# Kernel optimization log

Measured on AMD Instinct MI355X. Metric: run time of the kernel, lower is better.

Reference implementation:

```python
import jax, jax.numpy as jnp
import numpy as np

N_LVL = 127.0   # 8-bit symmetric: 2**(8-1) - 1
BN_EPS = 1e-5
PATCH = 16


def quant_act(x):
    """Per-tensor 8-bit symmetric quant-dequant (HAWQ-style QuantAct, dynamic range)."""
    scale = jnp.max(jnp.abs(x)) / N_LVL
    xq = jnp.clip(jnp.round(x / scale), -N_LVL, N_LVL) * scale
    return xq, scale


def setup_inputs() -> dict:
    key = jax.random.key(0)
    k0, k1, k2, k3, k4 = jax.random.split(key, 5)
    B, C, H = 128, 3, 224
    dim = 768
    x = jax.random.normal(k0, (B, C, H, H), jnp.float32)
    W = jax.random.normal(k1, (dim, C, PATCH, PATCH), jnp.float32) * 0.02
    b = jax.random.normal(k2, (dim,), jnp.float32) * 0.02
    gamma = jnp.ones((dim,), jnp.float32)
    beta = jnp.zeros((dim,), jnp.float32)
    run_mean = jax.random.normal(k3, (dim,), jnp.float32) * 0.1
    run_var = jax.random.uniform(k4, (dim,), jnp.float32, 0.5, 1.5)
    return {"x": x, "W": W, "b": b, "gamma": gamma, "beta": beta,
            "run_mean": run_mean, "run_var": run_var}


def reference(x, W, b, gamma, beta, run_mean, run_var):
    # --- quant_input ---
    x_q, pre_s = quant_act(x)                                   # [B,3,224,224], scalar
    # --- QuantConv2d: per-out-channel 8-bit symmetric weight quant ---
    w_scale = jnp.max(jnp.abs(W), axis=(1, 2, 3), keepdims=True) / N_LVL  # [dim,1,1,1]
    w_int = jnp.round(W / w_scale)
    x_int = x_q / pre_s                                         # integer-valued activations
    comb_s = w_scale[:, 0, 0, 0] * pre_s                        # [dim] conv output scale
    b_int = jnp.round(b / comb_s)
    y = jax.lax.conv_general_dilated(
        x_int, w_int, window_strides=(PATCH, PATCH), padding='VALID',
        dimension_numbers=('NCHW', 'OIHW', 'NCHW'))             # [B,768,14,14]
    y = (y + b_int[None, :, None, None]) * comb_s[None, :, None, None]
    # --- quant_act_conv ---
    y, _ = quant_act(y)
    # --- GELU (torch nn.GELU default: exact erf) ---
    y = jax.nn.gelu(y, approximate=False)
    # --- qact1 ---
    y, _ = quant_act(y)
    # --- BatchNorm2d (eval mode, running stats) ---
    inv = gamma / jnp.sqrt(run_var + BN_EPS)
    y = y * inv[None, :, None, None] + (beta - run_mean * inv)[None, :, None, None]
    # --- qact2 ---
    y, act_scale = quant_act(y)
    return y, act_scale
```

## Files before the change

kernel.cpp:

```cpp
#include <hip/hip_runtime.h>

#define TOT   19267584
#define MROWS 25088
#define KD    768
#define NPB   196
#define CHW   150528

typedef unsigned int uint;
typedef __attribute__((ext_vector_type(4))) int i32x4;

#define OFF_AQ   0ull
#define OFF_WQ   19267584ull
#define OFF_WSC  19857408ull
#define OFF_INV  19860480ull
#define OFF_SHF  19863552ull
#define OFF_CMN  19866624ull
#define OFF_CMX  19869696ull
#define OFF_SC   19872768ull

__device__ __forceinline__ float wave_max(float v) {
#pragma unroll
  for (int off = 32; off > 0; off >>= 1) v = fmaxf(v, __shfl_xor(v, off));
  return v;
}

__device__ __forceinline__ void block_max_atomic(float v, uint* dst) {
  __shared__ float red[4];
  v = wave_max(v);
  const int lane = threadIdx.x & 63, wv = threadIdx.x >> 6;
  if (lane == 0) red[wv] = v;
  __syncthreads();
  if (threadIdx.x == 0)
    atomicMax(dst, __float_as_uint(fmaxf(fmaxf(red[0], red[1]), fmaxf(red[2], red[3]))));
}

__global__ void k_maxabs(const float* __restrict__ x, uint* __restrict__ sc) {
  float m = 0.f;
  const float4* x4 = (const float4*)x;
  for (int i = blockIdx.x * blockDim.x + threadIdx.x; i < TOT / 4; i += gridDim.x * blockDim.x) {
    float4 v = x4[i];
    m = fmaxf(m, fmaxf(fmaxf(fabsf(v.x), fabsf(v.y)), fmaxf(fabsf(v.z), fabsf(v.w))));
  }
  block_max_atomic(m, sc + 0);
}

__global__ void k_wquant(const float* __restrict__ W, const float* __restrict__ gamma,
                         const float* __restrict__ beta, const float* __restrict__ rmean,
                         const float* __restrict__ rvar, signed char* __restrict__ wq,
                         float* __restrict__ wscale, float* __restrict__ inv_,
                         float* __restrict__ shf) {
  const int oc = blockIdx.x;
  const float* row = W + oc * KD;
  float m = 0.f;
  for (int k = threadIdx.x; k < KD; k += 256) m = fmaxf(m, fabsf(row[k]));
  __shared__ float red[4];
  m = wave_max(m);
  if ((threadIdx.x & 63) == 0) red[threadIdx.x >> 6] = m;
  __syncthreads();
  const float ws_ = fmaxf(fmaxf(red[0], red[1]), fmaxf(red[2], red[3])) / 127.0f;
  for (int k = threadIdx.x; k < KD; k += 256)
    wq[oc * KD + k] = (signed char)(int)rintf(row[k] / ws_);
  if (threadIdx.x == 0) {
    wscale[oc] = ws_;
    float iv = gamma[oc] / sqrtf(rvar[oc] + 1e-5f);
    inv_[oc] = iv;
    shf[oc] = __fsub_rn(beta[oc], __fmul_rn(rmean[oc], iv));
  }
}

__global__ void k_im2col(const float* __restrict__ x, const uint* __restrict__ sc,
                         signed char* __restrict__ aq) {
  const float ps = __uint_as_float(sc[0]) / 127.0f;
  char4* a4 = (char4*)aq;
  for (int u = blockIdx.x * blockDim.x + threadIdx.x; u < TOT / 4; u += gridDim.x * blockDim.x) {
    int p = u / 192;
    int k = (u - p * 192) * 4;
    int c = k >> 8;
    int r = k & 255;
    int kh = r >> 4, kw = r & 15;
    int b = p / NPB;
    int pp = p - b * NPB;
    int ph = pp / 14;
    int pw = pp - ph * 14;
    float4 v = *(const float4*)(x + (((b * 3 + c) * 224 + ph * 16 + kh) * 224 + pw * 16 + kw));
    char4 o;
    o.x = (signed char)(int)fminf(fmaxf(rintf(v.x / ps), -127.f), 127.f);
    o.y = (signed char)(int)fminf(fmaxf(rintf(v.y / ps), -127.f), 127.f);
    o.z = (signed char)(int)fminf(fmaxf(rintf(v.z / ps), -127.f), 127.f);
    o.w = (signed char)(int)fminf(fmaxf(rintf(v.w / ps), -127.f), 127.f);
    a4[u] = o;
  }
}

__device__ __forceinline__ void gl_lds16(const void* g, void* l) {
  __builtin_amdgcn_global_load_lds((const __attribute__((address_space(1))) void*)g,
                                   (__attribute__((address_space(3))) void*)l, 16, 0, 0);
}

__global__ __launch_bounds__(256) void k_gemm(const signed char* __restrict__ aq,
                                              const signed char* __restrict__ wq,
                                              const float* __restrict__ bias,
                                              const float* __restrict__ wscale,
                                              uint* __restrict__ sc,
                                              float* __restrict__ y) {
  __shared__ __align__(16) signed char lA[2][8192];
  __shared__ __align__(16) signed char lB[2][8192];
  const int tid = threadIdx.x, lane = tid & 63, wv = tid >> 6;
  const int bsw = (blockIdx.x & 7) * 147 + (blockIdx.x >> 3);
  const int bm = bsw / 6, bn = bsw - 6 * (bsw / 6);
  const int wr = wv >> 1, wc = wv & 1;
  const float ps = __uint_as_float(sc[0]) / 127.0f;

  const int ci0 = wv * 2, ci1 = wv * 2 + 1;
  const int rr0 = ci0 * 16 + (lane >> 2);
  const int rr1 = ci1 * 16 + (lane >> 2);
  const int bo = (lane & 3) * 16;
  const signed char* gA0 = aq + (size_t)(bm * 128 + rr0) * KD + bo;
  const signed char* gA1 = aq + (size_t)(bm * 128 + rr1) * KD + bo;
  const signed char* gB0 = wq + (size_t)(bn * 128 + rr0) * KD + bo;
  const signed char* gB1 = wq + (size_t)(bn * 128 + rr1) * KD + bo;

  i32x4 acc[4][4];
#pragma unroll
  for (int m = 0; m < 4; ++m)
#pragma unroll
    for (int n = 0; n < 4; ++n) acc[m][n] = (i32x4){0, 0, 0, 0};

  const int rbase = lane & 15;
  const int kg = (lane >> 4) * 16;

  gl_lds16(gA0, &lA[0][ci0 * 1024]);
  gl_lds16(gA1, &lA[0][ci1 * 1024]);
  gl_lds16(gB0, &lB[0][ci0 * 1024]);
  gl_lds16(gB1, &lB[0][ci1 * 1024]);
  __syncthreads();

  int cur = 0;
  for (int t = 0; t < 12; ++t) {
    if (t < 11) {
      const int kk = (t + 1) * 64;
      gl_lds16(gA0 + kk, &lA[cur ^ 1][ci0 * 1024]);
      gl_lds16(gA1 + kk, &lA[cur ^ 1][ci1 * 1024]);
      gl_lds16(gB0 + kk, &lB[cur ^ 1][ci0 * 1024]);
      gl_lds16(gB1 + kk, &lB[cur ^ 1][ci1 * 1024]);
    }
    i32x4 af[4], bfr[4];
#pragma unroll
    for (int m = 0; m < 4; ++m)
      af[m] = *(const i32x4*)&lA[cur][(wr * 64 + m * 16 + rbase) * 64 + kg];
#pragma unroll
    for (int n = 0; n < 4; ++n)
      bfr[n] = *(const i32x4*)&lB[cur][(wc * 64 + n * 16 + rbase) * 64 + kg];
#pragma unroll
    for (int m = 0; m < 4; ++m)
#pragma unroll
      for (int n = 0; n < 4; ++n)
        acc[m][n] = __builtin_amdgcn_mfma_i32_16x16x64_i8(af[m], bfr[n], acc[m][n], 0, 0, 0);
    __syncthreads();
    cur ^= 1;
  }

  float lmax = 0.f;
  const int prow = (lane >> 4) << 2;
#pragma unroll
  for (int n = 0; n < 4; ++n) {
    const int oc = bn * 128 + wc * 64 + n * 16 + rbase;
    const float comb = wscale[oc] * ps;
    const float bint = rintf(bias[oc] / comb);
#pragma unroll
    for (int m = 0; m < 4; ++m) {
      const int p0 = bm * 128 + wr * 64 + m * 16 + prow;
      const int img = p0 / 196;
      const int q = p0 - img * 196;
      float4 o;
      o.x = ((float)acc[m][n][0] + bint) * comb;
      o.y = ((float)acc[m][n][1] + bint) * comb;
      o.z = ((float)acc[m][n][2] + bint) * comb;
      o.w = ((float)acc[m][n][3] + bint) * comb;
      lmax = fmaxf(lmax, fmaxf(fmaxf(fabsf(o.x), fabsf(o.y)), fmaxf(fabsf(o.z), fabsf(o.w))));
      *(float4*)(y + (size_t)img * CHW + (size_t)oc * 196 + q) = o;
    }
  }
  block_max_atomic(lmax, sc + 1);
}

__global__ void k_gelu_chan(const float* __restrict__ y, const uint* __restrict__ sc,
                            signed char* __restrict__ k1, float* __restrict__ chmn,
                            float* __restrict__ chmx) {
  const int c = blockIdx.x;
  const float s1 = __uint_as_float(sc[1]) / 127.0f;
  __shared__ float tab[255];
  for (int t = threadIdx.x; t < 255; t += 256) {
    float y1 = (float)(t - 127) * s1;
    float e = erff(y1 * 0.70710678118654752f);
    tab[t] = (y1 * (e + 1.0f)) * 0.5f;
  }
  __syncthreads();
  float mn = 1e30f, mx = -1e30f;
  char4* k4 = (char4*)k1;
  for (int u = threadIdx.x; u < 6272; u += 256) {
    int img = u / 49, j = u - img * 49;
    size_t base4 = (size_t)img * (CHW / 4) + c * 49;
    float4 v = ((const float4*)y)[base4 + j];
    int a = (int)fminf(fmaxf(rintf(v.x / s1), -127.f), 127.f);
    int b = (int)fminf(fmaxf(rintf(v.y / s1), -127.f), 127.f);
    int cc = (int)fminf(fmaxf(rintf(v.z / s1), -127.f), 127.f);
    int d = (int)fminf(fmaxf(rintf(v.w / s1), -127.f), 127.f);
    char4 kk;
    kk.x = (signed char)a; kk.y = (signed char)b; kk.z = (signed char)cc; kk.w = (signed char)d;
    k4[base4 + j] = kk;
    float ga = tab[a + 127], gb = tab[b + 127], gc = tab[cc + 127], gd = tab[d + 127];
    mn = fminf(mn, fminf(fminf(ga, gb), fminf(gc, gd)));
    mx = fmaxf(mx, fmaxf(fmaxf(ga, gb), fmaxf(gc, gd)));
  }
  __shared__ float rmn[4], rmx[4];
#pragma unroll
  for (int off = 32; off > 0; off >>= 1) {
    mn = fminf(mn, __shfl_xor(mn, off));
    mx = fmaxf(mx, __shfl_xor(mx, off));
  }
  const int lane = threadIdx.x & 63, wv = threadIdx.x >> 6;
  if (lane == 0) { rmn[wv] = mn; rmx[wv] = mx; }
  __syncthreads();
  if (threadIdx.x == 0) {
    chmn[c] = fminf(fminf(rmn[0], rmn[1]), fminf(rmn[2], rmn[3]));
    chmx[c] = fmaxf(fmaxf(rmx[0], rmx[1]), fmaxf(rmx[2], rmx[3]));
  }
}

__global__ void k_scales(const float* __restrict__ chmn, const float* __restrict__ chmx,
                         const float* __restrict__ inv_, const float* __restrict__ shf,
                         uint* __restrict__ sc) {
  __shared__ float sred[4];
  __shared__ float s2sh;
  const int tid = threadIdx.x;
  float m2 = 0.f;
  for (int c = tid; c < 768; c += 256)
    m2 = fmaxf(m2, fmaxf(fabsf(chmn[c]), fabsf(chmx[c])));
  m2 = wave_max(m2);
  if ((tid & 63) == 0) sred[tid >> 6] = m2;
  __syncthreads();
  if (tid == 0) {
    float s2 = fmaxf(fmaxf(sred[0], sred[1]), fmaxf(sred[2], sred[3])) / 127.0f;
    s2sh = s2;
    sc[2] = __float_as_uint(s2);
  }
  __syncthreads();
  const float s2 = s2sh;
  float m4 = 0.f;
  for (int c = tid; c < 768; c += 256) {
    float iv = inv_[c], sh = shf[c];
    float a = fminf(fmaxf(rintf(chmn[c] / s2), -127.f), 127.f) * s2;
    float b = fminf(fmaxf(rintf(chmx[c] / s2), -127.f), 127.f) * s2;
    float ya = __fadd_rn(__fmul_rn(a, iv), sh);
    float yb = __fadd_rn(__fmul_rn(b, iv), sh);
    m4 = fmaxf(m4, fmaxf(fabsf(ya), fabsf(yb)));
  }
  m4 = wave_max(m4);
  __syncthreads();
  if ((tid & 63) == 0) sred[tid >> 6] = m4;
  __syncthreads();
  if (tid == 0)
    sc[3] = __float_as_uint(fmaxf(fmaxf(sred[0], sred[1]), fmaxf(sred[2], sred[3])) / 127.0f);
}

__global__ void k_final(const signed char* __restrict__ k1, const uint* __restrict__ sc,
                        const float* __restrict__ inv_, const float* __restrict__ shf,
                        float* __restrict__ out) {
  __shared__ float tab[255];
  const float s1 = __uint_as_float(sc[1]) / 127.0f;
  const float s2 = __uint_as_float(sc[2]);
  const float s3 = __uint_as_float(sc[3]);
  for (int t = threadIdx.x; t < 255; t += 256) {
    float y1 = (float)(t - 127) * s1;
    float e = erff(y1 * 0.70710678118654752f);
    float y2 = (y1 * (e + 1.0f)) * 0.5f;
    float q2 = fminf(fmaxf(rintf(y2 / s2), -127.f), 127.f);
    tab[t] = q2 * s2;
  }
  __syncthreads();
  for (int u = blockIdx.x * blockDim.x + threadIdx.x; u < TOT / 4; u += gridDim.x * blockDim.x) {
    int c = ((u * 4) / 196) % 768;
    float iv = inv_[c], sh = shf[c];
    char4 kk = ((const char4*)k1)[u];
    float a = __fadd_rn(__fmul_rn(tab[kk.x + 127], iv), sh);
    float b = __fadd_rn(__fmul_rn(tab[kk.y + 127], iv), sh);
    float cc = __fadd_rn(__fmul_rn(tab[kk.z + 127], iv), sh);
    float d = __fadd_rn(__fmul_rn(tab[kk.w + 127], iv), sh);
    float4 o;
    o.x = fminf(fmaxf(rintf(a / s3), -127.f), 127.f) * s3;
    o.y = fminf(fmaxf(rintf(b / s3), -127.f), 127.f) * s3;
    o.z = fminf(fmaxf(rintf(cc / s3), -127.f), 127.f) * s3;
    o.w = fminf(fmaxf(rintf(d / s3), -127.f), 127.f) * s3;
    ((float4*)out)[u] = o;
  }
  if (blockIdx.x == 0 && threadIdx.x == 0) out[TOT] = s3;
}

extern "C" void kernel_launch(void* const* d_in, const int* in_sizes, int n_in,
                              void* d_out, int out_size, void* d_ws, size_t ws_size,
                              hipStream_t stream) {
  const float* x     = (const float*)d_in[0];
  const float* W     = (const float*)d_in[1];
  const float* bias  = (const float*)d_in[2];
  const float* gamma = (const float*)d_in[3];
  const float* beta  = (const float*)d_in[4];
  const float* rmean = (const float*)d_in[5];
  const float* rvar  = (const float*)d_in[6];
  float* out = (float*)d_out;
  char* ws = (char*)d_ws;

  signed char* aq  = (signed char*)(ws + OFF_AQ);
  signed char* wq  = (signed char*)(ws + OFF_WQ);
  float* wsc  = (float*)(ws + OFF_WSC);
  float* inv_ = (float*)(ws + OFF_INV);
  float* shf  = (float*)(ws + OFF_SHF);
  float* cmn  = (float*)(ws + OFF_CMN);
  float* cmx  = (float*)(ws + OFF_CMX);
  uint*  sc   = (uint*)(ws + OFF_SC);
  signed char* k1 = (signed char*)(ws + OFF_AQ);

  hipMemsetAsync(sc, 0, 16, stream);
  k_maxabs<<<2048, 256, 0, stream>>>(x, sc);
  k_wquant<<<768, 256, 0, stream>>>(W, gamma, beta, rmean, rvar, wq, wsc, inv_, shf);
  k_im2col<<<2048, 256, 0, stream>>>(x, sc, aq);
  k_gemm<<<1176, 256, 0, stream>>>(aq, wq, bias, wsc, sc, out);
  k_gelu_chan<<<768, 256, 0, stream>>>(out, sc, k1, cmn, cmx);
  k_scales<<<1, 256, 0, stream>>>(cmn, cmx, inv_, shf, sc);
  k_final<<<2048, 256, 0, stream>>>(k1, sc, inv_, shf, out);
}
```

Measured before the change: 154.6 us.

## Flatten elementwise kernels, widen im2col stores, swizzle GEMM LDS, split per-channel GELU

Replaces the grid-stride loops in the max-abs, im2col and final kernels with one-shot grids where each thread loads four independent float4/char4 values, raising memory-level parallelism. Im2col now handles a whole 16-element row per thread and writes one 16-byte packed store. The GEMM XORs the 16-byte chunk offsets on both the global-to-LDS copy and the fragment read, to cut LDS bank conflicts. The GELU pass splits each channel across two blocks and merges per-channel min/max with order-preserving uint atomics, which needs a larger memset to clear them. Launch sizes are hard-coded to the exact tensor size, so nothing guards the bounds.

After: 172.7 us. +11.7%, slower.

```diff
diff --git a/kernel.cpp b/kernel.cpp
--- a/kernel.cpp
+++ b/kernel.cpp
@@ -5,6 +5,7 @@
 #define KD    768
 #define NPB   196
 #define CHW   150528
+#define STRD  1204224
 
 typedef unsigned int uint;
 typedef __attribute__((ext_vector_type(4))) int i32x4;
@@ -14,8 +15,8 @@
 #define OFF_WSC  19857408ull
 #define OFF_INV  19860480ull
 #define OFF_SHF  19863552ull
-#define OFF_CMN  19866624ull
-#define OFF_CMX  19869696ull
+#define OFF_EMN  19866624ull
+#define OFF_EMX  19869696ull
 #define OFF_SC   19872768ull
 
 __device__ __forceinline__ float wave_max(float v) {
@@ -34,13 +35,25 @@
     atomicMax(dst, __float_as_uint(fmaxf(fmaxf(red[0], red[1]), fmaxf(red[2], red[3]))));
 }
 
+__device__ __forceinline__ uint enc(float f) {
+  uint b = __float_as_uint(f);
+  return (b & 0x80000000u) ? ~b : (b | 0x80000000u);
+}
+__device__ __forceinline__ float dec(uint k) {
+  return __uint_as_float((k & 0x80000000u) ? (k & 0x7fffffffu) : ~k);
+}
+
 __global__ void k_maxabs(const float* __restrict__ x, uint* __restrict__ sc) {
-  float m = 0.f;
+  const int i = blockIdx.x * 256 + threadIdx.x;
   const float4* x4 = (const float4*)x;
-  for (int i = blockIdx.x * blockDim.x + threadIdx.x; i < TOT / 4; i += gridDim.x * blockDim.x) {
-    float4 v = x4[i];
-    m = fmaxf(m, fmaxf(fmaxf(fabsf(v.x), fabsf(v.y)), fmaxf(fabsf(v.z), fabsf(v.w))));
-  }
+  float4 v0 = x4[i];
+  float4 v1 = x4[i + STRD];
+  float4 v2 = x4[i + 2 * STRD];
+  float4 v3 = x4[i + 3 * STRD];
+  float m = fmaxf(fmaxf(fmaxf(fabsf(v0.x), fabsf(v0.y)), fmaxf(fabsf(v0.z), fabsf(v0.w))),
+                  fmaxf(fmaxf(fabsf(v1.x), fabsf(v1.y)), fmaxf(fabsf(v1.z), fabsf(v1.w))));
+  m = fmaxf(m, fmaxf(fmaxf(fabsf(v2.x), fabsf(v2.y)), fmaxf(fabsf(v2.z), fabsf(v2.w))));
+  m = fmaxf(m, fmaxf(fmaxf(fabsf(v3.x), fabsf(v3.y)), fmaxf(fabsf(v3.z), fabsf(v3.w))));
   block_max_atomic(m, sc + 0);
 }
 
@@ -71,25 +84,24 @@
 __global__ void k_im2col(const float* __restrict__ x, const uint* __restrict__ sc,
                          signed char* __restrict__ aq) {
   const float ps = __uint_as_float(sc[0]) / 127.0f;
-  char4* a4 = (char4*)aq;
-  for (int u = blockIdx.x * blockDim.x + threadIdx.x; u < TOT / 4; u += gridDim.x * blockDim.x) {
-    int p = u / 192;
-    int k = (u - p * 192) * 4;
-    int c = k >> 8;
-    int r = k & 255;
-    int kh = r >> 4, kw = r & 15;
-    int b = p / NPB;
-    int pp = p - b * NPB;
-    int ph = pp / 14;
-    int pw = pp - ph * 14;
-    float4 v = *(const float4*)(x + (((b * 3 + c) * 224 + ph * 16 + kh) * 224 + pw * 16 + kw));
-    char4 o;
-    o.x = (signed char)(int)fminf(fmaxf(rintf(v.x / ps), -127.f), 127.f);
-    o.y = (signed char)(int)fminf(fmaxf(rintf(v.y / ps), -127.f), 127.f);
-    o.z = (signed char)(int)fminf(fmaxf(rintf(v.z / ps), -127.f), 127.f);
-    o.w = (signed char)(int)fminf(fmaxf(rintf(v.w / ps), -127.f), 127.f);
-    a4[u] = o;
-  }
+  const int u = blockIdx.x * 256 + threadIdx.x;
+  const int p = u / 48, r = u - p * 48;
+  const int c = r >> 4, kh = r & 15;
+  const int b = p / NPB, pp = p - b * NPB;
+  const int ph = pp / 14, pw = pp - ph * 14;
+  const float* src = x + (((b * 3 + c) * 224 + ph * 16 + kh) * 224 + pw * 16);
+  float4 v0 = *(const float4*)(src);
+  float4 v1 = *(const float4*)(src + 4);
+  float4 v2 = *(const float4*)(src + 8);
+  float4 v3 = *(const float4*)(src + 12);
+#define Q8(v) ((int)fminf(fmaxf(rintf((v) / ps), -127.f), 127.f) & 255)
+  uint4 o;
+  o.x = Q8(v0.x) | (Q8(v0.y) << 8) | (Q8(v0.z) << 16) | ((uint)Q8(v0.w) << 24);
+  o.y = Q8(v1.x) | (Q8(v1.y) << 8) | (Q8(v1.z) << 16) | ((uint)Q8(v1.w) << 24);
+  o.z = Q8(v2.x) | (Q8(v2.y) << 8) | (Q8(v2.z) << 16) | ((uint)Q8(v2.w) << 24);
+  o.w = Q8(v3.x) | (Q8(v3.y) << 8) | (Q8(v3.z) << 16) | ((uint)Q8(v3.w) << 24);
+#undef Q8
+  *(uint4*)(aq + (size_t)p * KD + (r << 4)) = o;
 }
 
 __device__ __forceinline__ void gl_lds16(const void* g, void* l) {
@@ -114,7 +126,7 @@
   const int ci0 = wv * 2, ci1 = wv * 2 + 1;
   const int rr0 = ci0 * 16 + (lane >> 2);
   const int rr1 = ci1 * 16 + (lane >> 2);
-  const int bo = (lane & 3) * 16;
+  const int bo = (((lane & 3) ^ ((lane >> 2) & 3)) << 4);
   const signed char* gA0 = aq + (size_t)(bm * 128 + rr0) * KD + bo;
   const signed char* gA1 = aq + (size_t)(bm * 128 + rr1) * KD + bo;
   const signed char* gB0 = wq + (size_t)(bn * 128 + rr0) * KD + bo;
@@ -127,7 +139,7 @@
     for (int n = 0; n < 4; ++n) acc[m][n] = (i32x4){0, 0, 0, 0};
 
   const int rbase = lane & 15;
-  const int kg = (lane >> 4) * 16;
+  const int kg = (((lane >> 4) << 4)) ^ ((lane & 3) << 4);
 
   gl_lds16(gA0, &lA[0][ci0 * 1024]);
   gl_lds16(gA1, &lA[0][ci1 * 1024]);
@@ -185,9 +197,9 @@
 }
 
 __global__ void k_gelu_chan(const float* __restrict__ y, const uint* __restrict__ sc,
-                            signed char* __restrict__ k1, float* __restrict__ chmn,
-                            float* __restrict__ chmx) {
-  const int c = blockIdx.x;
+                            signed char* __restrict__ k1, uint* __restrict__ emn,
+                            uint* __restrict__ emx) {
+  const int c = blockIdx.x >> 1, half = blockIdx.x & 1;
   const float s1 = __uint_as_float(sc[1]) / 127.0f;
   __shared__ float tab[255];
   for (int t = threadIdx.x; t < 255; t += 256) {
@@ -197,46 +209,70 @@
   }
   __syncthreads();
   float mn = 1e30f, mx = -1e30f;
+  const float4* y4 = (const float4*)y;
   char4* k4 = (char4*)k1;
-  for (int u = threadIdx.x; u < 6272; u += 256) {
-    int img = u / 49, j = u - img * 49;
-    size_t base4 = (size_t)img * (CHW / 4) + c * 49;
-    float4 v = ((const float4*)y)[base4 + j];
-    int a = (int)fminf(fmaxf(rintf(v.x / s1), -127.f), 127.f);
-    int b = (int)fminf(fmaxf(rintf(v.y / s1), -127.f), 127.f);
-    int cc = (int)fminf(fmaxf(rintf(v.z / s1), -127.f), 127.f);
-    int d = (int)fminf(fmaxf(rintf(v.w / s1), -127.f), 127.f);
-    char4 kk;
-    kk.x = (signed char)a; kk.y = (signed char)b; kk.z = (signed char)cc; kk.w = (signed char)d;
-    k4[base4 + j] = kk;
-    float ga = tab[a + 127], gb = tab[b + 127], gc = tab[cc + 127], gd = tab[d + 127];
-    mn = fminf(mn, fminf(fminf(ga, gb), fminf(gc, gd)));
-    mx = fmaxf(mx, fmaxf(fmaxf(ga, gb), fmaxf(gc, gd)));
-  }
+  const int imgbase = half * 64;
+#define ADDR(u) ((size_t)(imgbase + (u) / 49) * (CHW / 4) + (size_t)c * 49 + ((u) - ((u) / 49) * 49))
+#define PROC(v, a4)                                                        \
+  {                                                                        \
+    int ia = (int)fminf(fmaxf(rintf((v).x / s1), -127.f), 127.f);          \
+    int ib = (int)fminf(fmaxf(rintf((v).y / s1), -127.f), 127.f);          \
+    int ic = (int)fminf(fmaxf(rintf((v).z / s1), -127.f), 127.f);          \
+    int id = (int)fminf(fmaxf(rintf((v).w / s1), -127.f), 127.f);          \
+    char4 kk;                                                              \
+    kk.x = (signed char)ia; kk.y = (signed char)ib;                        \
+    kk.z = (signed char)ic; kk.w = (signed char)id;                        \
+    k4[a4] = kk;                                                           \
+    float ga = tab[ia + 127], gb = tab[ib + 127];                          \
+    float gc = tab[ic + 127], gd = tab[id + 127];                          \
+    mn = fminf(mn, fminf(fminf(ga, gb), fminf(gc, gd)));                   \
+    mx = fmaxf(mx, fmaxf(fmaxf(ga, gb), fmaxf(gc, gd)));                   \
+  }
+  for (int r = 0; r < 3; ++r) {
+    const int u0 = threadIdx.x + r * 1024;
+    const size_t a0 = ADDR(u0), a1 = ADDR(u0 + 256), a2 = ADDR(u0 + 512), a3 = ADDR(u0 + 768);
+    float4 v0 = y4[a0];
+    float4 v1 = y4[a1];
+    float4 v2 = y4[a2];
+    float4 v3 = y4[a3];
+    PROC(v0, a0) PROC(v1, a1) PROC(v2, a2) PROC(v3, a3)
+  }
+  if (threadIdx.x < 64) {
+    const int u = 3072 + threadIdx.x;
+    const size_t a = ADDR(u);
+    float4 v = y4[a];
+    PROC(v, a)
+  }
+#undef PROC
+#undef ADDR
   __shared__ float rmn[4], rmx[4];
 #pragma unroll
   for (int off = 32; off > 0; off >>= 1) {
     mn = fminf(mn, __shfl_xor(mn, off));
     mx = fmaxf(mx, __shfl_xor(mx, off));
   }
-  const int lane = threadIdx.x & 63, wv = threadIdx.x >> 6;
-  if (lane == 0) { rmn[wv] = mn; rmx[wv] = mx; }
+  const int lane = threadIdx.x & 63, wvx = threadIdx.x >> 6;
+  if (lane == 0) { rmn[wvx] = mn; rmx[wvx] = mx; }
   __syncthreads();
   if (threadIdx.x == 0) {
-    chmn[c] = fminf(fminf(rmn[0], rmn[1]), fminf(rmn[2], rmn[3]));
-    chmx[c] = fmaxf(fmaxf(rmx[0], rmx[1]), fmaxf(rmx[2], rmx[3]));
-  }
-}
-
-__global__ void k_scales(const float* __restrict__ chmn, const float* __restrict__ chmx,
+    float bmn = fminf(fminf(rmn[0], rmn[1]), fminf(rmn[2], rmn[3]));
+    float bmx = fmaxf(fmaxf(rmx[0], rmx[1]), fmaxf(rmx[2], rmx[3]));
+    atomicMax(&emn[c], enc(-bmn));
+    atomicMax(&emx[c], enc(bmx));
+  }
+}
+
+__global__ void k_scales(const uint* __restrict__ emn, const uint* __restrict__ emx,
                          const float* __restrict__ inv_, const float* __restrict__ shf,
                          uint* __restrict__ sc) {
   __shared__ float sred[4];
   __shared__ float s2sh;
   const int tid = threadIdx.x;
   float m2 = 0.f;
-  for (int c = tid; c < 768; c += 256)
-    m2 = fmaxf(m2, fmaxf(fabsf(chmn[c]), fabsf(chmx[c])));
+  for (int c = tid; c < 768; c += 256) {
+    float mn = -dec(emn[c]), mx = dec(emx[c]);
+    m2 = fmaxf(m2, fmaxf(fabsf(mn), fabsf(mx)));
+  }
   m2 = wave_max(m2);
   if ((tid & 63) == 0) sred[tid >> 6] = m2;
   __syncthreads();
@@ -249,9 +285,10 @@
   const float s2 = s2sh;
   float m4 = 0.f;
   for (int c = tid; c < 768; c += 256) {
+    float mn = -dec(emn[c]), mx = dec(emx[c]);
     float iv = inv_[c], sh = shf[c];
-    float a = fminf(fmaxf(rintf(chmn[c] / s2), -127.f), 127.f) * s2;
-    float b = fminf(fmaxf(rintf(chmx[c] / s2), -127.f), 127.f) * s2;
+    float a = fminf(fmaxf(rintf(mn / s2), -127.f), 127.f) * s2;
+    float b = fminf(fmaxf(rintf(mx / s2), -127.f), 127.f) * s2;
     float ya = __fadd_rn(__fmul_rn(a, iv), sh);
     float yb = __fadd_rn(__fmul_rn(b, iv), sh);
     m4 = fmaxf(m4, fmaxf(fabsf(ya), fabsf(yb)));
@@ -279,21 +316,33 @@
     tab[t] = q2 * s2;
   }
   __syncthreads();
-  for (int u = blockIdx.x * blockDim.x + threadIdx.x; u < TOT / 4; u += gridDim.x * blockDim.x) {
-    int c = ((u * 4) / 196) % 768;
-    float iv = inv_[c], sh = shf[c];
-    char4 kk = ((const char4*)k1)[u];
-    float a = __fadd_rn(__fmul_rn(tab[kk.x + 127], iv), sh);
-    float b = __fadd_rn(__fmul_rn(tab[kk.y + 127], iv), sh);
-    float cc = __fadd_rn(__fmul_rn(tab[kk.z + 127], iv), sh);
-    float d = __fadd_rn(__fmul_rn(tab[kk.w + 127], iv), sh);
-    float4 o;
-    o.x = fminf(fmaxf(rintf(a / s3), -127.f), 127.f) * s3;
-    o.y = fminf(fmaxf(rintf(b / s3), -127.f), 127.f) * s3;
-    o.z = fminf(fmaxf(rintf(cc / s3), -127.f), 127.f) * s3;
-    o.w = fminf(fmaxf(rintf(d / s3), -127.f), 127.f) * s3;
-    ((float4*)out)[u] = o;
-  }
+  const int i = blockIdx.x * 256 + threadIdx.x;
+  const char4* k4 = (const char4*)k1;
+  char4 a0 = k4[i];
+  char4 a1 = k4[i + STRD];
+  char4 a2 = k4[i + 2 * STRD];
+  char4 a3 = k4[i + 3 * STRD];
+  float4* out4 = (float4*)out;
+#define FIN(kk, idx)                                                       \
+  {                                                                        \
+    int c = ((idx) / 49) % 768;                                            \
+    float iv = inv_[c], sh = shf[c];                                       \
+    float fa = __fadd_rn(__fmul_rn(tab[kk.x + 127], iv), sh);              \
+    float fb = __fadd_rn(__fmul_rn(tab[kk.y + 127], iv), sh);              \
+    float fc = __fadd_rn(__fmul_rn(tab[kk.z + 127], iv), sh);              \
+    float fd = __fadd_rn(__fmul_rn(tab[kk.w + 127], iv), sh);              \
+    float4 o;                                                              \
+    o.x = fminf(fmaxf(rintf(fa / s3), -127.f), 127.f) * s3;                \
+    o.y = fminf(fmaxf(rintf(fb / s3), -127.f), 127.f) * s3;                \
+    o.z = fminf(fmaxf(rintf(fc / s3), -127.f), 127.f) * s3;                \
+    o.w = fminf(fmaxf(rintf(fd / s3), -127.f), 127.f) * s3;                \
+    out4[idx] = o;                                                         \
+  }
+  FIN(a0, i)
+  FIN(a1, i + STRD)
+  FIN(a2, i + 2 * STRD)
+  FIN(a3, i + 3 * STRD)
+#undef FIN
   if (blockIdx.x == 0 && threadIdx.x == 0) out[TOT] = s3;
 }
 
@@ -315,17 +364,17 @@
   float* wsc  = (float*)(ws + OFF_WSC);
   float* inv_ = (float*)(ws + OFF_INV);
   float* shf  = (float*)(ws + OFF_SHF);
-  float* cmn  = (float*)(ws + OFF_CMN);
-  float* cmx  = (float*)(ws + OFF_CMX);
+  uint*  emn  = (uint*)(ws + OFF_EMN);
+  uint*  emx  = (uint*)(ws + OFF_EMX);
   uint*  sc   = (uint*)(ws + OFF_SC);
   signed char* k1 = (signed char*)(ws + OFF_AQ);
 
-  hipMemsetAsync(sc, 0, 16, stream);
-  k_maxabs<<<2048, 256, 0, stream>>>(x, sc);
+  hipMemsetAsync(ws + OFF_EMN, 0, 6160, stream);
+  k_maxabs<<<4704, 256, 0, stream>>>(x, sc);
   k_wquant<<<768, 256, 0, stream>>>(W, gamma, beta, rmean, rvar, wq, wsc, inv_, shf);
-  k_im2col<<<2048, 256, 0, stream>>>(x, sc, aq);
+  k_im2col<<<4704, 256, 0, stream>>>(x, sc, aq);
   k_gemm<<<1176, 256, 0, stream>>>(aq, wq, bias, wsc, sc, out);
-  k_gelu_chan<<<768, 256, 0, stream>>>(out, sc, k1, cmn, cmx);
-  k_scales<<<1, 256, 0, stream>>>(cmn, cmx, inv_, shf, sc);
-  k_final<<<2048, 256, 0, stream>>>(k1, sc, inv_, shf, out);
-}
+  k_gelu_chan<<<1536, 256, 0, stream>>>(out, sc, k1, emn, emx);
+  k_scales<<<1, 256, 0, stream>>>(emn, emx, inv_, shf, sc);
+  k_final<<<4704, 256, 0, stream>>>(k1, sc, inv_, shf, out);
+}
```
